# Kernel optimization log

Measured on AMD Instinct MI355X. Metric: run time of the kernel, lower is better.

## Reference

```python
import jax, jax.numpy as jnp
import numpy as np

N = 100000        # nodes
E_RAND = 1500000  # random edges (self loops appended -> E = 1.6M)
IN_DIM = 500
HID = 256
NCLASS = 50
K = 10


def setup_inputs() -> dict:
    key = jax.random.key(0)
    ks = jax.random.split(key, 8)
    feats = jax.random.normal(ks[0], (N, IN_DIM), dtype=jnp.float32)
    # edges: random + self loops (fit() adds self loops)
    src_r = jax.random.randint(ks[1], (E_RAND,), 0, N, dtype=jnp.int32)
    dst_r = jax.random.randint(ks[2], (E_RAND,), 0, N, dtype=jnp.int32)
    loop = jnp.arange(N, dtype=jnp.int32)
    src = jnp.concatenate([src_r, loop])
    dst = jnp.concatenate([dst_r, loop])
    # params (xavier-uniform-like scales)
    def xavier(k, shape):
        lim = np.sqrt(6.0 / (shape[0] + shape[1]))
        return jax.random.uniform(k, shape, jnp.float32, -lim, lim)
    W1 = xavier(ks[3], (IN_DIM, HID))
    b1 = jnp.zeros((HID,), jnp.float32)
    W2 = xavier(ks[4], (HID, NCLASS))
    b2 = jnp.zeros((NCLASS,), jnp.float32)
    s = xavier(ks[5], (NCLASS, 1))
    return {"feats": feats, "W1": W1, "b1": b1, "W2": W2, "b2": b2,
            "s": s, "src": src, "dst": dst}


def reference(feats, W1, b1, W2, b2, s, src, dst):
    # --- MLP (dropout is identity in eval / p=0) ---
    x = jax.nn.relu(feats @ W1 + b1)          # [N, HID]
    x = x @ W2 + b2                            # [N, NCLASS]
    # --- DAGNNConv: k-hop sym-normalized propagation ---
    deg = jax.ops.segment_sum(jnp.ones_like(dst, dtype=jnp.float32), dst,
                              num_segments=N)  # in-degrees
    norm = jnp.power(deg, -0.5)[:, None]       # [N, 1]
    results = [x]
    h = x
    for _ in range(K):
        h = h * norm
        h = jax.ops.segment_sum(h[src], dst, num_segments=N)  # copy_u + sum
        h = h * norm
        results.append(h)
    H = jnp.stack(results, axis=1)             # [N, K+1, C]
    S = jax.nn.sigmoid(jnp.einsum('nkc,co->nk', H, s))  # [N, K+1]
    out = jnp.einsum('nk,nkc->nc', S, H)       # [N, C]
    return out
```

## Files before the change

### kernel.cpp

```cpp
#include <hip/hip_runtime.h>
#include <hip/hip_bf16.h>
#include <math.h>

#define NN     100000
#define INDIM  500
#define HID    256
#define NCLASS 50
#define KHOPS  10
#define KPAD   512
#define CPAD   64

static inline size_t roundup256(size_t x) { return (x + 255) & ~(size_t)255; }

typedef __attribute__((ext_vector_type(8))) short bf16x8;
typedef __attribute__((ext_vector_type(4))) float f32x4;
typedef __attribute__((ext_vector_type(4))) short short4v;

__device__ inline short f2bf(float f) {
    union { float f; unsigned u; } v; v.f = f;
    unsigned r = v.u + 0x7FFFu + ((v.u >> 16) & 1u);
    return (short)(r >> 16);
}

__global__ void dagnn_zero2(int* __restrict__ a, int* __restrict__ b, int n) {
    int i = blockIdx.x * blockDim.x + threadIdx.x;
    if (i < n) { a[i] = 0; b[i] = 0; }
}

__global__ void dagnn_deg(const int* __restrict__ dst, int* __restrict__ degi, int E) {
    int e = blockIdx.x * blockDim.x + threadIdx.x;
    if (e < E) atomicAdd(&degi[dst[e]], 1);
}

__global__ void dagnn_norm(const int* __restrict__ degi, float* __restrict__ nrm, int n) {
    int i = blockIdx.x * blockDim.x + threadIdx.x;
    if (i < n) nrm[i] = rsqrtf((float)degi[i]);
}

__global__ void dagnn_scan(const int* __restrict__ degi, int* __restrict__ rowptr, int n) {
    __shared__ int wsum[16];
    __shared__ int carry_s;
    const int tid  = threadIdx.x;
    const int lane = tid & 63;
    const int wid  = tid >> 6;
    if (tid == 0) carry_s = 0;
    __syncthreads();
    for (int base = 0; base < n; base += 4096) {
        int i0 = base + tid * 4;
        int v0 = (i0 + 0 < n) ? degi[i0 + 0] : 0;
        int v1 = (i0 + 1 < n) ? degi[i0 + 1] : 0;
        int v2 = (i0 + 2 < n) ? degi[i0 + 2] : 0;
        int v3 = (i0 + 3 < n) ? degi[i0 + 3] : 0;
        int tsum = v0 + v1 + v2 + v3;
        int x = tsum;
        #pragma unroll
        for (int off = 1; off < 64; off <<= 1) {
            int t = __shfl_up(x, off);
            if (lane >= off) x += t;
        }
        if (lane == 63) wsum[wid] = x;
        __syncthreads();
        if (tid == 0) {
            int run = carry_s;
            #pragma unroll
            for (int w = 0; w < 16; ++w) { int t = wsum[w]; wsum[w] = run; run += t; }
            carry_s = run;
        }
        __syncthreads();
        int texcl = wsum[wid] + (x - tsum);
        if (i0 + 0 < n) rowptr[i0 + 0] = texcl;
        if (i0 + 1 < n) rowptr[i0 + 1] = texcl + v0;
        if (i0 + 2 < n) rowptr[i0 + 2] = texcl + v0 + v1;
        if (i0 + 3 < n) rowptr[i0 + 3] = texcl + v0 + v1 + v2;
        __syncthreads();
    }
    if (tid == 0) rowptr[n] = carry_s;
}

__global__ void dagnn_fill(const int* __restrict__ src, const int* __restrict__ dst,
                           const int* __restrict__ rowptr, int* __restrict__ fillc,
                           int* __restrict__ colidx, int E) {
    int e = blockIdx.x * blockDim.x + threadIdx.x;
    if (e >= E) return;
    int d = dst[e];
    int pos = rowptr[d] + atomicAdd(&fillc[d], 1);
    colidx[pos] = src[e];
}

__global__ void dagnn_w1t(const float* __restrict__ W1, short* __restrict__ W1t) {
    int idx = blockIdx.x * 256 + threadIdx.x;
    if (idx >= HID * KPAD) return;
    int n = idx >> 9;
    int k = idx & (KPAD - 1);
    float v = (k < INDIM) ? W1[(size_t)k * HID + n] : 0.f;
    W1t[idx] = f2bf(v);
}

__global__ void dagnn_w2t(const float* __restrict__ W2, short* __restrict__ W2t) {
    int idx = blockIdx.x * 256 + threadIdx.x;
    if (idx >= CPAD * HID) return;
    int n = idx >> 8;
    int k = idx & 255;
    float v = (n < NCLASS) ? W2[(size_t)k * NCLASS + n] : 0.f;
    W2t[idx] = f2bf(v);
}

#define G1_STRIDE 40
__global__ __launch_bounds__(512) void dagnn_gemm1_mfma(
        const float* __restrict__ A, const short* __restrict__ Bt,
        const float* __restrict__ bias, short* __restrict__ C, int M) {
    __shared__ __align__(16) short As[128 * G1_STRIDE];
    __shared__ __align__(16) short Bs[256 * G1_STRIDE];

    const int tid  = threadIdx.x;
    const int lane = tid & 63;
    const int wid  = tid >> 6;
    const int l16  = lane & 15;
    const int quad = lane >> 4;
    const int m_off = (wid & 1) * 64;
    const int n_off = (wid >> 1) * 64;
    const int row0  = blockIdx.x * 128;

    f32x4 acc[4][4] = {};

    for (int ks = 0; ks < KPAD / 32; ++ks) {
        const int k0 = ks * 32;
        #pragma unroll
        for (int it = 0; it < 2; ++it) {
            int slot = tid + it * 512;
            int m   = slot >> 3;
            int seg = slot & 7;
            int gm  = row0 + m;
            int gk  = k0 + seg * 4;
            float v0 = 0.f, v1 = 0.f, v2 = 0.f, v3 = 0.f;
            if (gm < M) {
                const float* ap = A + (size_t)gm * INDIM + gk;
                if (gk + 3 < INDIM) {
                    float4 f = *(const float4*)ap;
                    v0 = f.x; v1 = f.y; v2 = f.z; v3 = f.w;
                } else {
                    if (gk + 0 < INDIM) v0 = ap[0];
                    if (gk + 1 < INDIM) v1 = ap[1];
                    if (gk + 2 < INDIM) v2 = ap[2];
                    if (gk + 3 < INDIM) v3 = ap[3];
                }
            }
            short4v sv; sv.x = f2bf(v0); sv.y = f2bf(v1); sv.z = f2bf(v2); sv.w = f2bf(v3);
            *(short4v*)&As[m * G1_STRIDE + seg * 4] = sv;
        }
        #pragma unroll
        for (int it = 0; it < 2; ++it) {
            int slot = tid + it * 512;
            int n   = slot >> 2;
            int seg = slot & 3;
            bf16x8 b = *(const bf16x8*)(Bt + (size_t)n * KPAD + k0 + seg * 8);
            *(bf16x8*)&Bs[n * G1_STRIDE + seg * 8] = b;
        }
        __syncthreads();

        bf16x8 af[4], bf[4];
        #pragma unroll
        for (int mt = 0; mt < 4; ++mt)
            af[mt] = *(const bf16x8*)&As[(m_off + mt * 16 + l16) * G1_STRIDE + quad * 8];
        #pragma unroll
        for (int nt = 0; nt < 4; ++nt)
            bf[nt] = *(const bf16x8*)&Bs[(n_off + nt * 16 + l16) * G1_STRIDE + quad * 8];
        #pragma unroll
        for (int mt = 0; mt < 4; ++mt)
            #pragma unroll
            for (int nt = 0; nt < 4; ++nt)
                acc[mt][nt] = __builtin_amdgcn_mfma_f32_16x16x32_bf16(
                                  af[mt], bf[nt], acc[mt][nt], 0, 0, 0);
        __syncthreads();
    }

    #pragma unroll
    for (int nt = 0; nt < 4; ++nt) {
        int gc = n_off + nt * 16 + l16;
        float bb = bias[gc];
        #pragma unroll
        for (int mt = 0; mt < 4; ++mt) {
            #pragma unroll
            for (int r = 0; r < 4; ++r) {
                int gm = row0 + m_off + mt * 16 + quad * 4 + r;
                if (gm < M) {
                    float v = acc[mt][nt][r] + bb;
                    C[(size_t)gm * HID + gc] = f2bf(v > 0.f ? v : 0.f);
                }
            }
        }
    }
}

#define A2_STRIDE 72
#define B2_STRIDE 264
__global__ __launch_bounds__(256) void dagnn_mlp2_mfma(
        const short* __restrict__ hid, const short* __restrict__ W2t,
        const float* __restrict__ b2, const float* __restrict__ svec,
        const float* __restrict__ nrm,
        float* __restrict__ hs0, float* __restrict__ out, int M) {
    __shared__ __align__(16) short As[128 * A2_STRIDE];
    __shared__ __align__(16) short Bs[CPAD * B2_STRIDE];

    const int tid  = threadIdx.x;
    const int lane = tid & 63;
    const int wid  = tid >> 6;
    const int l16  = lane & 15;
    const int quad = lane >> 4;
    const int m_off = wid * 32;
    const int row0  = blockIdx.x * 128;

    #pragma unroll
    for (int it = 0; it < 8; ++it) {
        int slot = tid + it * 256;
        int n   = slot >> 5;
        int seg = slot & 31;
        bf16x8 b = *(const bf16x8*)(W2t + (size_t)n * HID + seg * 8);
        *(bf16x8*)&Bs[n * B2_STRIDE + seg * 8] = b;
    }

    f32x4 acc[2][4] = {};

    for (int ks = 0; ks < HID / 64; ++ks) {
        const int k0 = ks * 64;
        #pragma unroll
        for (int it = 0; it < 4; ++it) {
            int slot = tid + it * 256;
            int m   = slot >> 3;
            int seg = slot & 7;
            int gm  = row0 + m;
            bf16x8 v = {};
            if (gm < M) v = *(const bf16x8*)(hid + (size_t)gm * HID + k0 + seg * 8);
            *(bf16x8*)&As[m * A2_STRIDE + seg * 8] = v;
        }
        __syncthreads();

        #pragma unroll
        for (int ksub = 0; ksub < 2; ++ksub) {
            bf16x8 af[2], bf[4];
            #pragma unroll
            for (int mt = 0; mt < 2; ++mt)
                af[mt] = *(const bf16x8*)&As[(m_off + mt * 16 + l16) * A2_STRIDE
                                             + ksub * 32 + quad * 8];
            #pragma unroll
            for (int nt = 0; nt < 4; ++nt)
                bf[nt] = *(const bf16x8*)&Bs[(nt * 16 + l16) * B2_STRIDE
                                             + k0 + ksub * 32 + quad * 8];
            #pragma unroll
            for (int mt = 0; mt < 2; ++mt)
                #pragma unroll
                for (int nt = 0; nt < 4; ++nt)
                    acc[mt][nt] = __builtin_amdgcn_mfma_f32_16x16x32_bf16(
                                      af[mt], bf[nt], acc[mt][nt], 0, 0, 0);
        }
        __syncthreads();
    }

    float b2v[4], ssv[4];
    #pragma unroll
    for (int nt = 0; nt < 4; ++nt) {
        int gc = nt * 16 + l16;
        b2v[nt] = (gc < NCLASS) ? b2[gc]   : 0.f;
        ssv[nt] = (gc < NCLASS) ? svec[gc] : 0.f;
    }
    #pragma unroll
    for (int mt = 0; mt < 2; ++mt) {
        #pragma unroll
        for (int r = 0; r < 4; ++r) {
            int gm = row0 + m_off + mt * 16 + quad * 4 + r;
            float xv[4], q = 0.f;
            #pragma unroll
            for (int nt = 0; nt < 4; ++nt) {
                xv[nt] = acc[mt][nt][r] + b2v[nt];
                q += xv[nt] * ssv[nt];
            }
            #pragma unroll
            for (int off = 1; off < 16; off <<= 1) q += __shfl_xor(q, off);
            float S = 1.f / (1.f + __expf(-q));
            if (gm < M) {
                float nd = nrm[gm];
                #pragma unroll
                for (int nt = 0; nt < 4; ++nt) {
                    int gc = nt * 16 + l16;
                    hs0[(size_t)gm * CPAD + gc] = xv[nt] * nd;
                    if (gc < NCLASS) out[(size_t)gm * NCLASS + gc] = S * xv[nt];
                }
            }
        }
    }
}

__global__ __launch_bounds__(256) void dagnn_prop3(
        const float* __restrict__ hs, const float* __restrict__ nrm,
        const int* __restrict__ rowptr, const int* __restrict__ colidx,
        const float* __restrict__ svec, float* __restrict__ hs_next,
        float* __restrict__ out, int M) {
    const int lane = threadIdx.x & 63;
    const int wid  = threadIdx.x >> 6;
    const int d    = blockIdx.x * 4 + wid;
    if (d >= M) return;
    const int c   = lane;
    const int beg = rowptr[d];
    const int end = rowptr[d + 1];

    float acc = 0.f;
    int e = beg;
    for (; e + 8 <= end; e += 8) {
        int s0 = colidx[e + 0];
        int s1 = colidx[e + 1];
        int s2 = colidx[e + 2];
        int s3 = colidx[e + 3];
        int s4 = colidx[e + 4];
        int s5 = colidx[e + 5];
        int s6 = colidx[e + 6];
        int s7 = colidx[e + 7];
        float v0 = hs[(size_t)s0 * CPAD + c];
        float v1 = hs[(size_t)s1 * CPAD + c];
        float v2 = hs[(size_t)s2 * CPAD + c];
        float v3 = hs[(size_t)s3 * CPAD + c];
        float v4 = hs[(size_t)s4 * CPAD + c];
        float v5 = hs[(size_t)s5 * CPAD + c];
        float v6 = hs[(size_t)s6 * CPAD + c];
        float v7 = hs[(size_t)s7 * CPAD + c];
        acc += ((v0 + v1) + (v2 + v3)) + ((v4 + v5) + (v6 + v7));
    }
    for (; e < end; ++e) {
        int s = colidx[e];
        acc += hs[(size_t)s * CPAD + c];
    }

    float nd = nrm[d];
    float r = acc * nd;
    float ss = (c < NCLASS) ? svec[c] : 0.f;
    float p = r * ss;
    #pragma unroll
    for (int off = 32; off; off >>= 1) p += __shfl_xor(p, off);
    float S = 1.f / (1.f + __expf(-p));
    hs_next[(size_t)d * CPAD + c] = r * nd;
    if (c < NCLASS) out[(size_t)d * NCLASS + c] += S * r;
}

extern "C" void kernel_launch(void* const* d_in, const int* in_sizes, int n_in,
                              void* d_out, int out_size, void* d_ws, size_t ws_size,
                              hipStream_t stream) {
    const float* feats = (const float*)d_in[0];
    const float* W1    = (const float*)d_in[1];
    const float* b1    = (const float*)d_in[2];
    const float* W2    = (const float*)d_in[3];
    const float* b2    = (const float*)d_in[4];
    const float* svec  = (const float*)d_in[5];
    const int*   src   = (const int*)d_in[6];
    const int*   dst   = (const int*)d_in[7];
    float* out = (float*)d_out;

    const int M = in_sizes[0] / INDIM;
    const int E = in_sizes[6];

    char* p = (char*)d_ws;
    size_t off = 0;
    short* hid   = (short*)(p + off); off += roundup256((size_t)M * HID * 2);
    float* hsA   = (float*)(p + off); off += roundup256((size_t)M * CPAD * 4);
    float* hsB   = (float*)(p + off); off += roundup256((size_t)M * CPAD * 4);
    short* W1t   = (short*)(p + off); off += roundup256((size_t)HID * KPAD * 2);
    short* W2t   = (short*)(p + off); off += roundup256((size_t)CPAD * HID * 2);
    int*   degi  = (int*)  (p + off); off += roundup256((size_t)M * 4);
    float* nrm   = (float*)(p + off); off += roundup256((size_t)M * 4);
    int*   rowptr= (int*)  (p + off); off += roundup256((size_t)(M + 1) * 4);
    int*   fillc = (int*)  (p + off); off += roundup256((size_t)M * 4);
    int*   colidx= (int*)  (p + off); off += roundup256((size_t)E * 4);
    (void)ws_size;

    dagnn_zero2<<<(M + 255) / 256, 256, 0, stream>>>(degi, fillc, M);
    dagnn_deg<<<(E + 255) / 256, 256, 0, stream>>>(dst, degi, E);
    dagnn_norm<<<(M + 255) / 256, 256, 0, stream>>>(degi, nrm, M);
    dagnn_scan<<<1, 1024, 0, stream>>>(degi, rowptr, M);
    dagnn_fill<<<(E + 255) / 256, 256, 0, stream>>>(src, dst, rowptr, fillc, colidx, E);

    dagnn_w1t<<<(HID * KPAD + 255) / 256, 256, 0, stream>>>(W1, W1t);
    dagnn_w2t<<<(CPAD * HID + 255) / 256, 256, 0, stream>>>(W2, W2t);

    dagnn_gemm1_mfma<<<(M + 127) / 128, 512, 0, stream>>>(feats, W1t, b1, hid, M);
    dagnn_mlp2_mfma<<<(M + 127) / 128, 256, 0, stream>>>(hid, W2t, b2, svec, nrm,
                                                         hsA, out, M);

    float* hin = hsA;
    float* hout = hsB;
    for (int k = 0; k < KHOPS; ++k) {
        dagnn_prop3<<<(M + 3) / 4, 256, 0, stream>>>(hin, nrm, rowptr, colidx,
                                                     svec, hout, out, M);
        float* t = hin; hin = hout; hout = t;
    }
}
```

Measured before the change: 1.380 ms.

## Store propagation features as packed bf16 and prefetch GEMM1 tiles into registers

The propagated hidden state is now stored as packed bf16 pairs, 32 words per node instead of 64 floats. This halves the bytes gathered per edge in each of the ten hops. The propagation kernel splits each wave into two halves that handle alternating edges, then combines them with a shuffle, and it skips writing the next state on the last hop. GEMM1 now loads the next K tile into registers while the MFMAs run on the current tile. The risk is bf16 rounding that compounds across hops, and GEMM1 gains an extra barrier per step.

Result: faster. 1.176 ms (-14.7%).

```diff
diff --git a/kernel.cpp b/kernel.cpp
--- a/kernel.cpp
+++ b/kernel.cpp
@@ -20,6 +20,15 @@
     union { float f; unsigned u; } v; v.f = f;
     unsigned r = v.u + 0x7FFFu + ((v.u >> 16) & 1u);
     return (short)(r >> 16);
+}
+__device__ inline float bflo(unsigned u) {
+    union { unsigned u; float f; } v; v.u = u << 16; return v.f;
+}
+__device__ inline float bfhi(unsigned u) {
+    union { unsigned u; float f; } v; v.u = u & 0xFFFF0000u; return v.f;
+}
+__device__ inline unsigned packbf(float a, float b) {
+    return (unsigned)(unsigned short)f2bf(a) | ((unsigned)(unsigned short)f2bf(b) << 16);
 }
 
 __global__ void dagnn_zero2(int* __restrict__ a, int* __restrict__ b, int n) {
@@ -105,6 +114,15 @@
     W2t[idx] = f2bf(v);
 }
 
+__global__ void dagnn_sgate(const float* __restrict__ svec, float2* __restrict__ sg) {
+    int c = threadIdx.x;
+    if (c < 32) {
+        float x = (2 * c     < NCLASS) ? svec[2 * c]     : 0.f;
+        float y = (2 * c + 1 < NCLASS) ? svec[2 * c + 1] : 0.f;
+        sg[c] = make_float2(x, y);
+    }
+}
+
 #define G1_STRIDE 40
 __global__ __launch_bounds__(512) void dagnn_gemm1_mfma(
         const float* __restrict__ A, const short* __restrict__ Bt,
@@ -121,58 +139,74 @@
     const int n_off = (wid >> 1) * 64;
     const int row0  = blockIdx.x * 128;
 
+    int am[2], aseg[2], bn[2], bseg[2];
+    #pragma unroll
+    for (int it = 0; it < 2; ++it) {
+        int slot = tid + it * 512;
+        am[it] = slot >> 3; aseg[it] = slot & 7;
+        bn[it] = slot >> 2; bseg[it] = slot & 3;
+    }
+
+    float4 ra[2]; bf16x8 rb[2];
+
+    #define LOAD_TILE(k0)                                                     \
+        _Pragma("unroll")                                                     \
+        for (int it = 0; it < 2; ++it) {                                      \
+            int gm = row0 + am[it];                                           \
+            int gk = (k0) + aseg[it] * 4;                                     \
+            float4 f = {0.f, 0.f, 0.f, 0.f};                                  \
+            if (gm < M) {                                                     \
+                const float* ap = A + (size_t)gm * INDIM + gk;                \
+                if (gk + 3 < INDIM) f = *(const float4*)ap;                   \
+                else {                                                        \
+                    if (gk + 0 < INDIM) f.x = ap[0];                          \
+                    if (gk + 1 < INDIM) f.y = ap[1];                          \
+                    if (gk + 2 < INDIM) f.z = ap[2];                          \
+                    if (gk + 3 < INDIM) f.w = ap[3];                          \
+                }                                                             \
+            }                                                                 \
+            ra[it] = f;                                                       \
+            rb[it] = *(const bf16x8*)(Bt + (size_t)bn[it] * KPAD + (k0) + bseg[it] * 8); \
+        }
+
+    #define STORE_TILE()                                                      \
+        _Pragma("unroll")                                                     \
+        for (int it = 0; it < 2; ++it) {                                      \
+            short4v sv;                                                       \
+            sv.x = f2bf(ra[it].x); sv.y = f2bf(ra[it].y);                     \
+            sv.z = f2bf(ra[it].z); sv.w = f2bf(ra[it].w);                     \
+            *(short4v*)&As[am[it] * G1_STRIDE + aseg[it] * 4] = sv;           \
+            *(bf16x8*)&Bs[bn[it] * G1_STRIDE + bseg[it] * 8] = rb[it];        \
+        }
+
     f32x4 acc[4][4] = {};
 
+    LOAD_TILE(0)
+    STORE_TILE()
+    __syncthreads();
+
     for (int ks = 0; ks < KPAD / 32; ++ks) {
-        const int k0 = ks * 32;
-        #pragma unroll
-        for (int it = 0; it < 2; ++it) {
-            int slot = tid + it * 512;
-            int m   = slot >> 3;
-            int seg = slot & 7;
-            int gm  = row0 + m;
-            int gk  = k0 + seg * 4;
-            float v0 = 0.f, v1 = 0.f, v2 = 0.f, v3 = 0.f;
-            if (gm < M) {
-                const float* ap = A + (size_t)gm * INDIM + gk;
-                if (gk + 3 < INDIM) {
-                    float4 f = *(const float4*)ap;
-                    v0 = f.x; v1 = f.y; v2 = f.z; v3 = f.w;
-                } else {
-                    if (gk + 0 < INDIM) v0 = ap[0];
-                    if (gk + 1 < INDIM) v1 = ap[1];
-                    if (gk + 2 < INDIM) v2 = ap[2];
-                    if (gk + 3 < INDIM) v3 = ap[3];
-                }
-            }
-            short4v sv; sv.x = f2bf(v0); sv.y = f2bf(v1); sv.z = f2bf(v2); sv.w = f2bf(v3);
-            *(short4v*)&As[m * G1_STRIDE + seg * 4] = sv;
-        }
-        #pragma unroll
-        for (int it = 0; it < 2; ++it) {
-            int slot = tid + it * 512;
-            int n   = slot >> 2;
-            int seg = slot & 3;
-            bf16x8 b = *(const bf16x8*)(Bt + (size_t)n * KPAD + k0 + seg * 8);
-            *(bf16x8*)&Bs[n * G1_STRIDE + seg * 8] = b;
-        }
-        __syncthreads();
-
-        bf16x8 af[4], bf[4];
+        if (ks + 1 < KPAD / 32) { LOAD_TILE((ks + 1) * 32) }
+
+        bf16x8 af[4], bfr[4];
         #pragma unroll
         for (int mt = 0; mt < 4; ++mt)
             af[mt] = *(const bf16x8*)&As[(m_off + mt * 16 + l16) * G1_STRIDE + quad * 8];
         #pragma unroll
         for (int nt = 0; nt < 4; ++nt)
-            bf[nt] = *(const bf16x8*)&Bs[(n_off + nt * 16 + l16) * G1_STRIDE + quad * 8];
+            bfr[nt] = *(const bf16x8*)&Bs[(n_off + nt * 16 + l16) * G1_STRIDE + quad * 8];
         #pragma unroll
         for (int mt = 0; mt < 4; ++mt)
             #pragma unroll
             for (int nt = 0; nt < 4; ++nt)
                 acc[mt][nt] = __builtin_amdgcn_mfma_f32_16x16x32_bf16(
-                                  af[mt], bf[nt], acc[mt][nt], 0, 0, 0);
-        __syncthreads();
-    }
+                                  af[mt], bfr[nt], acc[mt][nt], 0, 0, 0);
+        __syncthreads();
+        if (ks + 1 < KPAD / 32) { STORE_TILE() }
+        __syncthreads();
+    }
+    #undef LOAD_TILE
+    #undef STORE_TILE
 
     #pragma unroll
     for (int nt = 0; nt < 4; ++nt) {
@@ -198,7 +232,7 @@
         const short* __restrict__ hid, const short* __restrict__ W2t,
         const float* __restrict__ b2, const float* __restrict__ svec,
         const float* __restrict__ nrm,
-        float* __restrict__ hs0, float* __restrict__ out, int M) {
+        unsigned* __restrict__ hs0, float* __restrict__ out, int M) {
     __shared__ __align__(16) short As[128 * A2_STRIDE];
     __shared__ __align__(16) short Bs[CPAD * B2_STRIDE];
 
@@ -237,21 +271,21 @@
 
         #pragma unroll
         for (int ksub = 0; ksub < 2; ++ksub) {
-            bf16x8 af[2], bf[4];
+            bf16x8 af[2], bfr[4];
             #pragma unroll
             for (int mt = 0; mt < 2; ++mt)
                 af[mt] = *(const bf16x8*)&As[(m_off + mt * 16 + l16) * A2_STRIDE
                                              + ksub * 32 + quad * 8];
             #pragma unroll
             for (int nt = 0; nt < 4; ++nt)
-                bf[nt] = *(const bf16x8*)&Bs[(nt * 16 + l16) * B2_STRIDE
-                                             + k0 + ksub * 32 + quad * 8];
+                bfr[nt] = *(const bf16x8*)&Bs[(nt * 16 + l16) * B2_STRIDE
+                                              + k0 + ksub * 32 + quad * 8];
             #pragma unroll
             for (int mt = 0; mt < 2; ++mt)
                 #pragma unroll
                 for (int nt = 0; nt < 4; ++nt)
                     acc[mt][nt] = __builtin_amdgcn_mfma_f32_16x16x32_bf16(
-                                      af[mt], bf[nt], acc[mt][nt], 0, 0, 0);
+                                      af[mt], bfr[nt], acc[mt][nt], 0, 0, 0);
         }
         __syncthreads();
     }
@@ -277,12 +311,15 @@
             #pragma unroll
             for (int off = 1; off < 16; off <<= 1) q += __shfl_xor(q, off);
             float S = 1.f / (1.f + __expf(-q));
-            if (gm < M) {
-                float nd = nrm[gm];
-                #pragma unroll
-                for (int nt = 0; nt < 4; ++nt) {
-                    int gc = nt * 16 + l16;
-                    hs0[(size_t)gm * CPAD + gc] = xv[nt] * nd;
+            float nd = (gm < M) ? nrm[gm] : 0.f;
+            #pragma unroll
+            for (int nt = 0; nt < 4; ++nt) {
+                int gc = nt * 16 + l16;
+                float hv = xv[nt] * nd;
+                float hp = __shfl_xor(hv, 1);
+                if (gm < M) {
+                    if (!(l16 & 1))
+                        hs0[(size_t)gm * 32 + nt * 8 + (l16 >> 1)] = packbf(hv, hp);
                     if (gc < NCLASS) out[(size_t)gm * NCLASS + gc] = S * xv[nt];
                 }
             }
@@ -290,54 +327,61 @@
     }
 }
 
-__global__ __launch_bounds__(256) void dagnn_prop3(
-        const float* __restrict__ hs, const float* __restrict__ nrm,
+__global__ __launch_bounds__(256) void dagnn_prop4(
+        const unsigned* __restrict__ hs, const float* __restrict__ nrm,
         const int* __restrict__ rowptr, const int* __restrict__ colidx,
-        const float* __restrict__ svec, float* __restrict__ hs_next,
-        float* __restrict__ out, int M) {
+        const float2* __restrict__ sgate, unsigned* __restrict__ hs_next,
+        float* __restrict__ out, int M, int write_next) {
     const int lane = threadIdx.x & 63;
     const int wid  = threadIdx.x >> 6;
     const int d    = blockIdx.x * 4 + wid;
     if (d >= M) return;
-    const int c   = lane;
-    const int beg = rowptr[d];
-    const int end = rowptr[d + 1];
-
-    float acc = 0.f;
+    const int half = lane >> 5;
+    const int c    = lane & 31;
+    const int beg = rowptr[d], end = rowptr[d + 1];
+
+    float a0 = 0.f, a1 = 0.f;
     int e = beg;
     for (; e + 8 <= end; e += 8) {
-        int s0 = colidx[e + 0];
-        int s1 = colidx[e + 1];
-        int s2 = colidx[e + 2];
-        int s3 = colidx[e + 3];
-        int s4 = colidx[e + 4];
-        int s5 = colidx[e + 5];
-        int s6 = colidx[e + 6];
-        int s7 = colidx[e + 7];
-        float v0 = hs[(size_t)s0 * CPAD + c];
-        float v1 = hs[(size_t)s1 * CPAD + c];
-        float v2 = hs[(size_t)s2 * CPAD + c];
-        float v3 = hs[(size_t)s3 * CPAD + c];
-        float v4 = hs[(size_t)s4 * CPAD + c];
-        float v5 = hs[(size_t)s5 * CPAD + c];
-        float v6 = hs[(size_t)s6 * CPAD + c];
-        float v7 = hs[(size_t)s7 * CPAD + c];
-        acc += ((v0 + v1) + (v2 + v3)) + ((v4 + v5) + (v6 + v7));
-    }
-    for (; e < end; ++e) {
+        int s0 = colidx[e + half + 0];
+        int s1 = colidx[e + half + 2];
+        int s2 = colidx[e + half + 4];
+        int s3 = colidx[e + half + 6];
+        unsigned u0 = hs[(size_t)s0 * 32 + c];
+        unsigned u1 = hs[(size_t)s1 * 32 + c];
+        unsigned u2 = hs[(size_t)s2 * 32 + c];
+        unsigned u3 = hs[(size_t)s3 * 32 + c];
+        a0 += (bflo(u0) + bflo(u1)) + (bflo(u2) + bflo(u3));
+        a1 += (bfhi(u0) + bfhi(u1)) + (bfhi(u2) + bfhi(u3));
+    }
+    for (; e + 2 <= end; e += 2) {
+        int s = colidx[e + half];
+        unsigned u = hs[(size_t)s * 32 + c];
+        a0 += bflo(u); a1 += bfhi(u);
+    }
+    if (e < end && half == 0) {
         int s = colidx[e];
-        acc += hs[(size_t)s * CPAD + c];
-    }
+        unsigned u = hs[(size_t)s * 32 + c];
+        a0 += bflo(u); a1 += bfhi(u);
+    }
+    a0 += __shfl_xor(a0, 32);
+    a1 += __shfl_xor(a1, 32);
 
     float nd = nrm[d];
-    float r = acc * nd;
-    float ss = (c < NCLASS) ? svec[c] : 0.f;
-    float p = r * ss;
-    #pragma unroll
-    for (int off = 32; off; off >>= 1) p += __shfl_xor(p, off);
+    float r0 = a0 * nd, r1 = a1 * nd;
+    float2 g = sgate[c];
+    float p = r0 * g.x + r1 * g.y;
+    #pragma unroll
+    for (int off = 16; off; off >>= 1) p += __shfl_xor(p, off);
     float S = 1.f / (1.f + __expf(-p));
-    hs_next[(size_t)d * CPAD + c] = r * nd;
-    if (c < NCLASS) out[(size_t)d * NCLASS + c] += S * r;
+    if (half == 0) {
+        if (write_next) hs_next[(size_t)d * 32 + c] = packbf(r0 * nd, r1 * nd);
+        int ch = 2 * c;
+        if (ch < NCLASS) {
+            out[(size_t)d * NCLASS + ch]     += S * r0;
+            out[(size_t)d * NCLASS + ch + 1] += S * r1;
+        }
+    }
 }
 
 extern "C" void kernel_launch(void* const* d_in, const int* in_sizes, int n_in,
@@ -358,16 +402,17 @@
 
     char* p = (char*)d_ws;
     size_t off = 0;
-    short* hid   = (short*)(p + off); off += roundup256((size_t)M * HID * 2);
-    float* hsA   = (float*)(p + off); off += roundup256((size_t)M * CPAD * 4);
-    float* hsB   = (float*)(p + off); off += roundup256((size_t)M * CPAD * 4);
-    short* W1t   = (short*)(p + off); off += roundup256((size_t)HID * KPAD * 2);
-    short* W2t   = (short*)(p + off); off += roundup256((size_t)CPAD * HID * 2);
-    int*   degi  = (int*)  (p + off); off += roundup256((size_t)M * 4);
-    float* nrm   = (float*)(p + off); off += roundup256((size_t)M * 4);
-    int*   rowptr= (int*)  (p + off); off += roundup256((size_t)(M + 1) * 4);
-    int*   fillc = (int*)  (p + off); off += roundup256((size_t)M * 4);
-    int*   colidx= (int*)  (p + off); off += roundup256((size_t)E * 4);
+    short*    hid   = (short*)   (p + off); off += roundup256((size_t)M * HID * 2);
+    unsigned* hsA   = (unsigned*)(p + off); off += roundup256((size_t)M * 32 * 4);
+    unsigned* hsB   = (unsigned*)(p + off); off += roundup256((size_t)M * 32 * 4);
+    short*    W1t   = (short*)   (p + off); off += roundup256((size_t)HID * KPAD * 2);
+    short*    W2t   = (short*)   (p + off); off += roundup256((size_t)CPAD * HID * 2);
+    float2*   sgate = (float2*)  (p + off); off += roundup256(32 * sizeof(float2));
+    int*      degi  = (int*)     (p + off); off += roundup256((size_t)M * 4);
+    float*    nrm   = (float*)   (p + off); off += roundup256((size_t)M * 4);
+    int*      rowptr= (int*)     (p + off); off += roundup256((size_t)(M + 1) * 4);
+    int*      fillc = (int*)     (p + off); off += roundup256((size_t)M * 4);
+    int*      colidx= (int*)     (p + off); off += roundup256((size_t)E * 4);
     (void)ws_size;
 
     dagnn_zero2<<<(M + 255) / 256, 256, 0, stream>>>(degi, fillc, M);
@@ -378,16 +423,18 @@
 
     dagnn_w1t<<<(HID * KPAD + 255) / 256, 256, 0, stream>>>(W1, W1t);
     dagnn_w2t<<<(CPAD * HID + 255) / 256, 256, 0, stream>>>(W2, W2t);
+    dagnn_sgate<<<1, 32, 0, stream>>>(svec, sgate);
 
     dagnn_gemm1_mfma<<<(M + 127) / 128, 512, 0, stream>>>(feats, W1t, b1, hid, M);
     dagnn_mlp2_mfma<<<(M + 127) / 128, 256, 0, stream>>>(hid, W2t, b2, svec, nrm,
                                                          hsA, out, M);
 
-    float* hin = hsA;
-    float* hout = hsB;
+    unsigned* hin = hsA;
+    unsigned* hout = hsB;
     for (int k = 0; k < KHOPS; ++k) {
-        dagnn_prop3<<<(M + 3) / 4, 256, 0, stream>>>(hin, nrm, rowptr, colidx,
-                                                     svec, hout, out, M);
-        float* t = hin; hin = hout; hout = t;
-    }
-}
+        dagnn_prop4<<<(M + 3) / 4, 256, 0, stream>>>(hin, nrm, rowptr, colidx,
+                                                     sgate, hout, out, M,
+                                                     k < KHOPS - 1);
+        unsigned* t = hin; hin = hout; hout = t;
+    }
+}
```
